# Kernel tuning notes

Measured on AMD Instinct MI355X. Metric: run time of the kernel, lower is better.

Reference implementation:

```python
import jax, jax.numpy as jnp
import numpy as np

N_NODES = 100000
N_EDGES = 1600000
N_GRAPHS = 512
IN_F, H1, H2 = 128, 128, 256
N_GROUPS, N_FAM = 16, 10


def setup_inputs() -> dict:
    key = jax.random.key(0)
    ks = jax.random.split(key, 8)
    x = jax.random.normal(ks[0], (N_NODES, IN_F), dtype=jnp.float32)
    edge_index = jax.random.randint(ks[1], (2, N_EDGES), 0, N_NODES, dtype=jnp.int64)
    batch = jnp.sort(jax.random.randint(ks[2], (N_NODES,), 0, N_GRAPHS, dtype=jnp.int64))
    W1 = jax.random.normal(ks[3], (IN_F, H1), dtype=jnp.float32) / np.sqrt(IN_F)
    b1 = jnp.zeros((H1,), dtype=jnp.float32)
    W2 = jax.random.normal(ks[4], (H1, H2), dtype=jnp.float32) / np.sqrt(H1)
    b2 = jnp.zeros((H2,), dtype=jnp.float32)
    Wg = jax.random.normal(ks[5], (H2, N_GROUPS), dtype=jnp.float32) / np.sqrt(H2)
    bg = jnp.zeros((N_GROUPS,), dtype=jnp.float32)
    Wf = jax.random.normal(ks[6], (N_GROUPS, H2, N_FAM), dtype=jnp.float32) / np.sqrt(H2)
    bf = jnp.zeros((N_GROUPS, N_FAM), dtype=jnp.float32)
    return {"x": x, "edge_index": edge_index, "batch": batch,
            "W1": W1, "b1": b1, "W2": W2, "b2": b2,
            "Wg": Wg, "bg": bg, "Wf": Wf, "bf": bf}


def gcn_conv(x, W, b, src, dst, num_nodes):
    # PyG GCNConv: add self-loops, symmetric normalization, scatter-add aggregation.
    xw = x @ W  # [N, out]
    deg = jax.ops.segment_sum(jnp.ones((src.shape[0],), x.dtype), dst,
                              num_segments=num_nodes) + 1.0  # +1 self-loop
    dinv = jax.lax.rsqrt(deg)
    coef = dinv[src] * dinv[dst]            # [E]
    msg = xw[src] * coef[:, None]           # gather + scale (memory-bound)
    agg = jax.ops.segment_sum(msg, dst, num_segments=num_nodes)
    agg = agg + xw * (dinv * dinv)[:, None]  # self-loop contribution
    return agg + b


def reference(x, edge_index, batch, W1, b1, W2, b2, Wg, bg, Wf, bf):
    src, dst = edge_index[0], edge_index[1]
    h = jax.nn.relu(gcn_conv(x, W1, b1, src, dst, N_NODES))
    # dropout p=0.5 is identity in eval mode
    h = gcn_conv(h, W2, b2, src, dst, N_NODES)
    # global mean pool over graphs
    sums = jax.ops.segment_sum(h, batch, num_segments=N_GRAPHS)       # [G, H2]
    cnts = jax.ops.segment_sum(jnp.ones((N_NODES,), h.dtype), batch,
                               num_segments=N_GRAPHS)
    pooled = sums / jnp.maximum(cnts, 1.0)[:, None]
    group_logits = pooled @ Wg + bg                                   # [G, num_groups]
    family_logits = jnp.einsum('bd,gdf->gbf', pooled, Wf) + bf[:, None, :]
    return group_logits, family_logits
```

## Files before the change

### kernel.cpp

```cpp
#include <hip/hip_runtime.h>

#define NN 100000
#define NE 1600000
#define NGR 512
#define KF 128
#define H2F 256
#define NGRP 16
#define NFAM 10

#define CH 128
#define NCHUNK ((NN + CH - 1) / CH)
#define PT 6656
#define NT ((NE + PT - 1) / PT)
#define PREPB_BLKS 64
#define GBB ((NN + 255) / 256)

#define NSPLIT 8
#define SRCMASK 0x1FFFF

typedef __attribute__((ext_vector_type(8))) short short8;
typedef __attribute__((ext_vector_type(4))) float floatx4;
typedef __attribute__((ext_vector_type(2))) float floatx2;

__device__ __forceinline__ unsigned short f2bf(float f) {
  unsigned u = __float_as_uint(f);
  unsigned r = (u + 0x7fff + ((u >> 16) & 1)) >> 16;
  return (unsigned short)r;
}
__device__ __forceinline__ unsigned short pk_fp8(float a, float b) {
  return (unsigned short)__builtin_amdgcn_cvt_pk_fp8_f32(a, b, 0, false);
}
__device__ __forceinline__ floatx2 unpk_fp8(unsigned short u) {
  return __builtin_amdgcn_cvt_pk_f32_fp8((int)u, false);
}


__global__ __launch_bounds__(256) void k_histprep(const int* __restrict__ ei,
                                                  const int* __restrict__ batch,
                                                  int* __restrict__ tot,
                                                  int* __restrict__ gb,
                                                  const float* __restrict__ W,
                                                  unsigned short* __restrict__ Bp) {
  __shared__ int lh[NCHUNK];
  int tid = threadIdx.x;
  if (blockIdx.x >= NT + PREPB_BLKS) {
    int n = (blockIdx.x - NT - PREPB_BLKS) * 256 + tid;
    if (n >= NN) return;
    int b0 = batch[n];
    if (n == 0) {
      for (int g = 0; g <= b0; ++g) gb[g] = 0;
    }
    int b1 = (n + 1 < NN) ? batch[n + 1] : NGR;
    for (int g = b0 + 1; g <= b1; ++g) gb[g] = n + 1;
    return;
  }
  if (blockIdx.x >= NT) {
    int idx = (blockIdx.x - NT) * 256 + tid;
    int j = idx & 7;
    int l = (idx >> 3) & 63;
    int rest = idx >> 9;
    int nc = rest & 7;
    int kc = rest >> 3;
    int k = kc * 32 + (l >> 4) * 8 + j;
    int nn = nc * 16 + (l & 15);
    Bp[idx] = f2bf(W[k * KF + nn]);
    return;
  }
  for (int g = tid; g < NCHUNK; g += 256) lh[g] = 0;
  __syncthreads();
  int base = blockIdx.x * PT;
  int nv = min(PT, NE - base);
  for (int i = tid; i < nv; i += 256) atomicAdd(&lh[ei[NE + base + i] >> 7], 1);
  __syncthreads();
  for (int g = tid; g < NCHUNK; g += 256) {
    int v = lh[g];
    if (v) atomicAdd(&tot[g], v);
  }
}


__global__ __launch_bounds__(256) void k_scantot(const int* __restrict__ tot,
                                                 int* __restrict__ cbase,
                                                 int* __restrict__ cursor) {
  __shared__ int ssc[256];
  int tid = threadIdx.x;
  int v4[4]; int loc = 0;
#pragma unroll
  for (int j = 0; j < 4; ++j) {
    int idx = tid * 4 + j;
    v4[j] = (idx < NCHUNK) ? tot[idx] : 0;
    loc += v4[j];
  }
  ssc[tid] = loc;
  __syncthreads();
  for (int off = 1; off < 256; off <<= 1) {
    int val = (tid >= off) ? ssc[tid - off] : 0;
    __syncthreads();
    ssc[tid] += val;
    __syncthreads();
  }
  int excl = ssc[tid] - loc;
#pragma unroll
  for (int j = 0; j < 4; ++j) {
    int idx = tid * 4 + j;
    if (idx < NCHUNK) { cbase[idx] = excl; cursor[idx] = excl; }
    excl += v4[j];
  }
  if (tid == 255) cbase[NCHUNK] = excl;
}


__global__ __launch_bounds__(256) void k_pscatter(const int* __restrict__ ei,
                                                  int* __restrict__ cursor,
                                                  int* __restrict__ erec) {
  __shared__ int stage[PT];
  __shared__ unsigned short stagec[PT];
  __shared__ int lstart[NCHUNK];
  __shared__ int lrun[NCHUNK];
  __shared__ int gbase[NCHUNK];
  __shared__ int ssc[256];
  int t0 = blockIdx.x, tid = threadIdx.x;
  for (int g = tid; g < NCHUNK; g += 256) lrun[g] = 0;
  __syncthreads();
  int base = t0 * PT;
  int nv = min(PT, NE - base);
  for (int i = tid; i < nv; i += 256) atomicAdd(&lrun[ei[NE + base + i] >> 7], 1);
  __syncthreads();
  int v4[4]; int loc = 0;
#pragma unroll
  for (int j = 0; j < 4; ++j) {
    int idx = tid * 4 + j;
    v4[j] = (idx < NCHUNK) ? lrun[idx] : 0;
    loc += v4[j];
  }
  ssc[tid] = loc;
  __syncthreads();
  for (int off = 1; off < 256; off <<= 1) {
    int val = (tid >= off) ? ssc[tid - off] : 0;
    __syncthreads();
    ssc[tid] += val;
    __syncthreads();
  }
  int excl = ssc[tid] - loc;
#pragma unroll
  for (int j = 0; j < 4; ++j) {
    int idx = tid * 4 + j;
    if (idx < NCHUNK) lstart[idx] = excl;
    excl += v4[j];
  }
  __syncthreads();
  for (int g = tid; g < NCHUNK; g += 256) {
    int cnt = ((g + 1 < NCHUNK) ? lstart[g + 1] : nv) - lstart[g];
    gbase[g] = cnt ? atomicAdd(&cursor[g], cnt) : 0;
    lrun[g] = lstart[g];
  }
  __syncthreads();
  for (int i = tid; i < nv; i += 256) {
    int s = ei[base + i], d = ei[NE + base + i];
    int g = d >> 7;
    int pos = atomicAdd(&lrun[g], 1);
    stage[pos] = ((d & (CH - 1)) << 17) | s;
    stagec[pos] = (unsigned short)g;
  }
  __syncthreads();
  for (int j = tid; j < nv; j += 256) {
    int g = stagec[j];
    erec[gbase[g] + (j - lstart[g])] = stage[j];
  }
}


__global__ __launch_bounds__(256) void k_sort(const int* __restrict__ erec,
                                              const int* __restrict__ cbase,
                                              int* __restrict__ esrc,
                                              int* __restrict__ rowptr,
                                              float* __restrict__ dinv) {
  __shared__ int hist[CH];
  __shared__ int lrun[CH];
  __shared__ int sc[256];
  const int c = blockIdx.x, tid = threadIdx.x;
  const int e0 = cbase[c], e1 = cbase[c + 1];
  const int nv = e1 - e0;
  if (tid < CH) hist[tid] = 0;
  __syncthreads();
  for (int i = tid; i < nv; i += 256) atomicAdd(&hist[(erec[e0 + i] >> 17) & (CH - 1)], 1);
  __syncthreads();
  int deg = (tid < CH) ? hist[tid] : 0;
  sc[tid] = deg;
  __syncthreads();
  for (int off = 1; off < 256; off <<= 1) {
    int val = (tid >= off) ? sc[tid - off] : 0;
    __syncthreads();
    sc[tid] += val;
    __syncthreads();
  }
  int excl = sc[tid] - deg;
  int node = c * CH + tid;
  if (tid < CH) {
    lrun[tid] = excl;
    if (node < NN) {
      rowptr[node] = e0 + excl;
      dinv[node] = rsqrtf((float)(deg + 1));
    } else if (node == NN) {
      rowptr[NN] = e0 + excl;
    }
  }
  __syncthreads();
  for (int i = tid; i < nv; i += 256) {
    int r = erec[e0 + i];
    int pos = atomicAdd(&lrun[(r >> 17) & (CH - 1)], 1);
    esrc[e0 + pos] = r & SRCMASK;
  }
}


__global__ __launch_bounds__(256) void k_gemm_mfma(const float* __restrict__ A,
                                                   const unsigned short* __restrict__ Bp,
                                                   const float* __restrict__ dinv,
                                                   unsigned short* __restrict__ C) {
  constexpr int K = 128;
  constexpr int NCH = KF / 16;
  const int wv = blockIdx.x * 4 + (threadIdx.x >> 6);
  const int row0 = wv * 16;
  if (row0 >= NN) return;
  const int lane = threadIdx.x & 63;
  const int m = lane & 15;
  const int q = lane >> 4;

  floatx4 acc[NCH];
#pragma unroll
  for (int i = 0; i < NCH; ++i) acc[i] = (floatx4){0.f, 0.f, 0.f, 0.f};

  const int arow = row0 + m;
#pragma unroll
  for (int kc = 0; kc < 4; ++kc) {
    const float* ap = A + (size_t)arow * K + kc * 32 + q * 8;
    float4 f0 = *(const float4*)ap;
    float4 f1 = *(const float4*)(ap + 4);
    short8 af;
    af[0] = (short)f2bf(f0.x); af[1] = (short)f2bf(f0.y);
    af[2] = (short)f2bf(f0.z); af[3] = (short)f2bf(f0.w);
    af[4] = (short)f2bf(f1.x); af[5] = (short)f2bf(f1.y);
    af[6] = (short)f2bf(f1.z); af[7] = (short)f2bf(f1.w);
    const unsigned short* bp = Bp + (size_t)kc * NCH * 512;
#pragma unroll
    for (int nc = 0; nc < NCH; ++nc) {
      short8 bfr = *(const short8*)(bp + (size_t)nc * 512 + lane * 8);
      acc[nc] = __builtin_amdgcn_mfma_f32_16x16x32_bf16(af, bfr, acc[nc], 0, 0, 0);
    }
  }

  float ds[4];
#pragma unroll
  for (int r = 0; r < 4; ++r) ds[r] = dinv[row0 + q * 4 + r];
#pragma unroll
  for (int nc = 0; nc < 4; ++nc) {
#pragma unroll
    for (int r = 0; r < 4; ++r) {
      int row = row0 + q * 4 + r;
      C[(size_t)row * 64 + nc * 16 + m] =
          pk_fp8(acc[nc][r] * ds[r], acc[nc + 4][r] * ds[r]);
    }
  }
}


__global__ __launch_bounds__(128) void k_agg1(const unsigned short* __restrict__ p,
                                              const float* __restrict__ bias,
                                              const int* __restrict__ rowptr,
                                              const int* __restrict__ esrc,
                                              const float* __restrict__ dinv,
                                              unsigned short* __restrict__ outp) {
  const int n = blockIdx.x * 2 + (threadIdx.x >> 6);
  const int t = threadIdx.x & 63;
  const int u = t & 31;
  const int half = t >> 5;
  const unsigned* __restrict__ prow = (const unsigned*)p;

  float a0 = 0.f, a1 = 0.f, a2 = 0.f, a3 = 0.f;

  if (half == 0) {
    unsigned v = prow[((unsigned)n << 5) + u];
    floatx2 lo = unpk_fp8((unsigned short)(v & 0xffffu));
    floatx2 hi = unpk_fp8((unsigned short)(v >> 16));
    a0 = lo.x; a1 = lo.y; a2 = hi.x; a3 = hi.y;
  }

  const int r0 = rowptr[n];
  const int r1 = rowptr[n + 1];
  int i = r0;

#define PAIR_TIER(NP)                                                  \
  for (; i + 2 * (NP) <= r1; i += 2 * (NP)) {                          \
    const int ib = i + half;                                           \
    unsigned s[NP];                                                    \
    _Pragma("unroll") for (int j = 0; j < (NP); ++j)                   \
        s[j] = (unsigned)esrc[ib + 2 * j];                             \
    unsigned v[NP];                                                    \
    _Pragma("unroll") for (int j = 0; j < (NP); ++j)                   \
        v[j] = prow[(s[j] << 5) + u];                                  \
    _Pragma("unroll") for (int j = 0; j < (NP); ++j) {                 \
      floatx2 lo = unpk_fp8((unsigned short)(v[j] & 0xffffu));         \
      floatx2 hi = unpk_fp8((unsigned short)(v[j] >> 16));             \
      a0 += lo.x; a1 += lo.y; a2 += hi.x; a3 += hi.y;                  \
    }                                                                  \
  }

  PAIR_TIER(8)
  PAIR_TIER(4)
  PAIR_TIER(2)
  PAIR_TIER(1)
#undef PAIR_TIER

  if (i < r1 && half == 0) {
    unsigned s = (unsigned)esrc[i];
    unsigned v = prow[(s << 5) + u];
    floatx2 lo = unpk_fp8((unsigned short)(v & 0xffffu));
    floatx2 hi = unpk_fp8((unsigned short)(v >> 16));
    a0 += lo.x; a1 += lo.y; a2 += hi.x; a3 += hi.y;
  }

  a0 += __shfl_down(a0, 32, 64);
  a1 += __shfl_down(a1, 32, 64);
  a2 += __shfl_down(a2, 32, 64);
  a3 += __shfl_down(a3, 32, 64);

  if (half == 0) {
    const float dn = dinv[n];
    float2 blo = *(const float2*)(bias + 2 * u);
    float2 bhi = *(const float2*)(bias + 64 + 2 * u);
    float x0 = fmaxf(fmaf(dn, a0, blo.x), 0.f) * dn;
    float x1 = fmaxf(fmaf(dn, a1, bhi.x), 0.f) * dn;
    float x2 = fmaxf(fmaf(dn, a2, blo.y), 0.f) * dn;
    float x3 = fmaxf(fmaf(dn, a3, bhi.y), 0.f) * dn;
    unsigned lo = pk_fp8(x0, x1);
    unsigned hi = pk_fp8(x2, x3);
    ((unsigned*)outp)[((unsigned)n << 5) + u] = lo | (hi << 16);
  }
}


__global__ __launch_bounds__(256) void k_aggpart(const unsigned short* __restrict__ p,
                                                 const int* __restrict__ gb,
                                                 const int* __restrict__ rowptr,
                                                 const int* __restrict__ esrc,
                                                 const float* __restrict__ dinv,
                                                 float* __restrict__ pooled) {
  __shared__ float sacc[4][128];
  const int g = blockIdx.x / NSPLIT;
  const int part = blockIdx.x % NSPLIT;
  const int tid = threadIdx.x;
  const int start = gb[g], end = gb[g + 1];
  const int wv = tid >> 6, t = tid & 63, u = t & 31, half = t >> 5;
  const unsigned* __restrict__ prow = (const unsigned*)p;

  float a0 = 0.f, a1 = 0.f, a2 = 0.f, a3 = 0.f;

  const int nlen = end - start;
  const int nper = (nlen + NSPLIT - 1) / NSPLIT;
  const int ns = min(start + part * nper, end);
  const int ne = min(ns + nper, end);

  for (int n = ns + wv; n < ne; n += 4) {
    float t0, t1, t2, t3;
    if (half == 0) {
      unsigned v = prow[((unsigned)n << 5) + u];
      floatx2 lo = unpk_fp8((unsigned short)(v & 0xffffu));
      floatx2 hi = unpk_fp8((unsigned short)(v >> 16));
      t0 = lo.x; t1 = lo.y; t2 = hi.x; t3 = hi.y;
    } else {
      t0 = 0.f; t1 = 0.f; t2 = 0.f; t3 = 0.f;
    }
    const int r0 = rowptr[n];
    const int r1 = rowptr[n + 1];
    int i = r0;

#define PAIR_TIER(NP)                                                  \
    for (; i + 2 * (NP) <= r1; i += 2 * (NP)) {                        \
      const int ib = i + half;                                         \
      unsigned s[NP];                                                  \
      _Pragma("unroll") for (int j = 0; j < (NP); ++j)                 \
          s[j] = (unsigned)esrc[ib + 2 * j];                           \
      unsigned v[NP];                                                  \
      _Pragma("unroll") for (int j = 0; j < (NP); ++j)                 \
          v[j] = prow[(s[j] << 5) + u];                                \
      _Pragma("unroll") for (int j = 0; j < (NP); ++j) {               \
        floatx2 lo = unpk_fp8((unsigned short)(v[j] & 0xffffu));       \
        floatx2 hi = unpk_fp8((unsigned short)(v[j] >> 16));           \
        t0 += lo.x; t1 += lo.y; t2 += hi.x; t3 += hi.y;                \
      }                                                                \
    }

    PAIR_TIER(8)
    PAIR_TIER(4)
    PAIR_TIER(2)
    PAIR_TIER(1)
#undef PAIR_TIER

    if (i < r1 && half == 0) {
      unsigned s = (unsigned)esrc[i];
      unsigned v = prow[(s << 5) + u];
      floatx2 lo = unpk_fp8((unsigned short)(v & 0xffffu));
      floatx2 hi = unpk_fp8((unsigned short)(v >> 16));
      t0 += lo.x; t1 += lo.y; t2 += hi.x; t3 += hi.y;
    }

    const float dn = dinv[n];
    a0 = fmaf(dn, t0, a0); a1 = fmaf(dn, t1, a1);
    a2 = fmaf(dn, t2, a2); a3 = fmaf(dn, t3, a3);
  }

  a0 += __shfl_down(a0, 32, 64);
  a1 += __shfl_down(a1, 32, 64);
  a2 += __shfl_down(a2, 32, 64);
  a3 += __shfl_down(a3, 32, 64);
  if (half == 0) {
    sacc[wv][2 * u] = a0;
    sacc[wv][2 * u + 1] = a2;
    sacc[wv][2 * u + 64] = a1;
    sacc[wv][2 * u + 65] = a3;
  }
  __syncthreads();
  if (tid < KF) {
    float v = sacc[0][tid] + sacc[1][tid] + sacc[2][tid] + sacc[3][tid];
    atomicAdd(&pooled[(size_t)g * KF + tid], v);
  }
}


__global__ __launch_bounds__(256) void k_heads(const float* __restrict__ pooled,
                                               const int* __restrict__ gb,
                                               const float* __restrict__ W2,
                                               const float* __restrict__ b2,
                                               const float* __restrict__ Wg,
                                               const float* __restrict__ bg,
                                               const float* __restrict__ Wf,
                                               const float* __restrict__ bfb,
                                               float* __restrict__ out) {
  __shared__ float pr[KF];
  __shared__ float pp[H2F];
  const int g = blockIdx.x;
  const int tid = threadIdx.x;
  if (tid < KF) {
    float c = fmaxf((float)(gb[g + 1] - gb[g]), 1.f);
    pr[tid] = pooled[(size_t)g * KF + tid] / c;
  }
  __syncthreads();
  float acc = b2[tid];
#pragma unroll 8
  for (int d = 0; d < KF; ++d) acc = fmaf(pr[d], W2[d * H2F + tid], acc);
  pp[tid] = acc;
  __syncthreads();
  if (tid < NGRP) {
    float a = bg[tid];
    for (int d = 0; d < H2F; ++d) a = fmaf(pp[d], Wg[d * NGRP + tid], a);
    out[g * NGRP + tid] = a;
  } else if (tid >= 64 && tid < 64 + NGRP * NFAM) {
    int uu = tid - 64;
    int gg = uu / NFAM;
    int ff = uu % NFAM;
    float a = bfb[gg * NFAM + ff];
    for (int d = 0; d < H2F; ++d) a = fmaf(pp[d], Wf[(gg * H2F + d) * NFAM + ff], a);
    out[NGR * NGRP + (size_t)gg * NGR * NFAM + g * NFAM + ff] = a;
  }
}


extern "C" void kernel_launch(void* const* d_in, const int* in_sizes, int n_in,
                              void* d_out, int out_size, void* d_ws, size_t ws_size,
                              hipStream_t stream) {
  const float* x    = (const float*)d_in[0];
  const int*   ei   = (const int*)d_in[1];
  const int*   batch= (const int*)d_in[2];
  const float* W1   = (const float*)d_in[3];
  const float* b1   = (const float*)d_in[4];
  const float* W2   = (const float*)d_in[5];
  const float* b2   = (const float*)d_in[6];
  const float* Wg   = (const float*)d_in[7];
  const float* bg   = (const float*)d_in[8];
  const float* Wf   = (const float*)d_in[9];
  const float* bfb  = (const float*)d_in[10];
  float* out = (float*)d_out;

  char* w = (char*)d_ws;
  auto take = [&](size_t bytes) {
    char* p = w;
    w += (bytes + 255) & ~(size_t)255;
    return (void*)p;
  };
  int*   tot   = (int*)take((size_t)NCHUNK * 4);
  float* pooled= (float*)take((size_t)NGR * KF * 4);
  int*   gb    = (int*)take((size_t)(NGR + 1) * 4);
  int*   cbase = (int*)take((size_t)(NCHUNK + 1) * 4);
  int*   cursor= (int*)take((size_t)NCHUNK * 4);
  int*   erec  = (int*)take((size_t)NE * 4);
  int*   esrc  = (int*)take((size_t)NE * 4);
  int*   rowptr= (int*)take((size_t)(NN + 1) * 4);
  float* dinv  = (float*)take((size_t)NN * 4);
  unsigned short* Bp1 = (unsigned short*)take((size_t)KF * KF * 2);
  unsigned short* xw1 = (unsigned short*)take((size_t)NN * 64 * 2);
  unsigned short* h1  = (unsigned short*)take((size_t)NN * 64 * 2);

  size_t zbytes = (size_t)((char*)pooled - (char*)tot) + (size_t)NGR * KF * 4;
  hipMemsetAsync(tot, 0, zbytes, stream);

  k_histprep<<<NT + PREPB_BLKS + GBB, 256, 0, stream>>>(ei, batch, tot, gb, W1, Bp1);
  k_scantot<<<1, 256, 0, stream>>>(tot, cbase, cursor);
  k_pscatter<<<NT, 256, 0, stream>>>(ei, cursor, erec);
  k_sort<<<NCHUNK, 256, 0, stream>>>(erec, cbase, esrc, rowptr, dinv);

  k_gemm_mfma<<<1563, 256, 0, stream>>>(x, Bp1, dinv, xw1);

  k_agg1<<<NN / 2, 128, 0, stream>>>(xw1, b1, rowptr, esrc, dinv, h1);
  k_aggpart<<<NGR * NSPLIT, 256, 0, stream>>>(h1, gb, rowptr, esrc, dinv, pooled);
  k_heads<<<NGR, 256, 0, stream>>>(pooled, gb, W2, b2, Wg, bg, Wf, bfb, out);
}
```

Before: 292.1 us.

## Compute degrees early and co-launch GEMM with partition scatter

Per-node in-degrees are now counted with global atomics in the histogram kernel, and dinv is computed in the scan kernel instead of in the sort kernel. Because dinv is ready sooner, the first-layer MFMA GEMM no longer has to wait for the sort. It is merged into the partition-scatter launch as extra blocks, so GEMM work overlaps the scatter and one kernel launch is removed. The cost is 1.6M extra global atomics on a 100K-entry degree array and a larger memset. The GEMM blocks also now carry the scatter kernel's large shared-memory footprint, which may lower their occupancy.

```diff
diff --git a/kernel.cpp b/kernel.cpp
--- a/kernel.cpp
+++ b/kernel.cpp
@@ -14,6 +14,7 @@
 #define NT ((NE + PT - 1) / PT)
 #define PREPB_BLKS 64
 #define GBB ((NN + 255) / 256)
+#define GEMMB 1563
 
 #define NSPLIT 8
 #define SRCMASK 0x1FFFF
@@ -38,6 +39,7 @@
 __global__ __launch_bounds__(256) void k_histprep(const int* __restrict__ ei,
                                                   const int* __restrict__ batch,
                                                   int* __restrict__ tot,
+                                                  int* __restrict__ nodedeg,
                                                   int* __restrict__ gb,
                                                   const float* __restrict__ W,
                                                   unsigned short* __restrict__ Bp) {
@@ -70,7 +72,11 @@
   __syncthreads();
   int base = blockIdx.x * PT;
   int nv = min(PT, NE - base);
-  for (int i = tid; i < nv; i += 256) atomicAdd(&lh[ei[NE + base + i] >> 7], 1);
+  for (int i = tid; i < nv; i += 256) {
+    int d = ei[NE + base + i];
+    atomicAdd(&lh[d >> 7], 1);
+    atomicAdd(&nodedeg[d], 1);
+  }
   __syncthreads();
   for (int g = tid; g < NCHUNK; g += 256) {
     int v = lh[g];
@@ -79,11 +85,18 @@
 }
 
 
-__global__ __launch_bounds__(256) void k_scantot(const int* __restrict__ tot,
-                                                 int* __restrict__ cbase,
-                                                 int* __restrict__ cursor) {
+__global__ __launch_bounds__(256) void k_scandinv(const int* __restrict__ tot,
+                                                  int* __restrict__ cbase,
+                                                  int* __restrict__ cursor,
+                                                  const int* __restrict__ nodedeg,
+                                                  float* __restrict__ dinv) {
+  int tid = threadIdx.x;
+  if (blockIdx.x > 0) {
+    int n = (blockIdx.x - 1) * 256 + tid;
+    if (n < NN) dinv[n] = rsqrtf((float)(nodedeg[n] + 1));
+    return;
+  }
   __shared__ int ssc[256];
-  int tid = threadIdx.x;
   int v4[4]; int loc = 0;
 #pragma unroll
   for (int j = 0; j < 4; ++j) {
@@ -110,16 +123,70 @@
 }
 
 
-__global__ __launch_bounds__(256) void k_pscatter(const int* __restrict__ ei,
-                                                  int* __restrict__ cursor,
-                                                  int* __restrict__ erec) {
+__global__ __launch_bounds__(256) void k_pscgemm(const int* __restrict__ ei,
+                                                 int* __restrict__ cursor,
+                                                 int* __restrict__ erec,
+                                                 const float* __restrict__ A,
+                                                 const unsigned short* __restrict__ Bp,
+                                                 const float* __restrict__ dinv,
+                                                 unsigned short* __restrict__ C) {
   __shared__ int stage[PT];
   __shared__ unsigned short stagec[PT];
   __shared__ int lstart[NCHUNK];
   __shared__ int lrun[NCHUNK];
   __shared__ int gbase[NCHUNK];
   __shared__ int ssc[256];
-  int t0 = blockIdx.x, tid = threadIdx.x;
+  const int tid = threadIdx.x;
+
+  if (blockIdx.x >= NT) {
+    constexpr int K = 128;
+    constexpr int NCH = KF / 16;
+    const int wv = (blockIdx.x - NT) * 4 + (tid >> 6);
+    const int row0 = wv * 16;
+    if (row0 >= NN) return;
+    const int lane = tid & 63;
+    const int m = lane & 15;
+    const int q = lane >> 4;
+
+    floatx4 acc[NCH];
+#pragma unroll
+    for (int i = 0; i < NCH; ++i) acc[i] = (floatx4){0.f, 0.f, 0.f, 0.f};
+
+    const int arow = row0 + m;
+#pragma unroll
+    for (int kc = 0; kc < 4; ++kc) {
+      const float* ap = A + (size_t)arow * K + kc * 32 + q * 8;
+      float4 f0 = *(const float4*)ap;
+      float4 f1 = *(const float4*)(ap + 4);
+      short8 af;
+      af[0] = (short)f2bf(f0.x); af[1] = (short)f2bf(f0.y);
+      af[2] = (short)f2bf(f0.z); af[3] = (short)f2bf(f0.w);
+      af[4] = (short)f2bf(f1.x); af[5] = (short)f2bf(f1.y);
+      af[6] = (short)f2bf(f1.z); af[7] = (short)f2bf(f1.w);
+      const unsigned short* bp = Bp + (size_t)kc * NCH * 512;
+#pragma unroll
+      for (int nc = 0; nc < NCH; ++nc) {
+        short8 bfr = *(const short8*)(bp + (size_t)nc * 512 + lane * 8);
+        acc[nc] = __builtin_amdgcn_mfma_f32_16x16x32_bf16(af, bfr, acc[nc], 0, 0, 0);
+      }
+    }
+
+    float ds[4];
+#pragma unroll
+    for (int r = 0; r < 4; ++r) ds[r] = dinv[row0 + q * 4 + r];
+#pragma unroll
+    for (int nc = 0; nc < 4; ++nc) {
+#pragma unroll
+      for (int r = 0; r < 4; ++r) {
+        int row = row0 + q * 4 + r;
+        C[(size_t)row * 64 + nc * 16 + m] =
+            pk_fp8(acc[nc][r] * ds[r], acc[nc + 4][r] * ds[r]);
+      }
+    }
+    return;
+  }
+
+  int t0 = blockIdx.x;
   for (int g = tid; g < NCHUNK; g += 256) lrun[g] = 0;
   __syncthreads();
   int base = t0 * PT;
@@ -173,8 +240,7 @@
 __global__ __launch_bounds__(256) void k_sort(const int* __restrict__ erec,
                                               const int* __restrict__ cbase,
                                               int* __restrict__ esrc,
-                                              int* __restrict__ rowptr,
-                                              float* __restrict__ dinv) {
+                                              int* __restrict__ rowptr) {
   __shared__ int hist[CH];
   __shared__ int lrun[CH];
   __shared__ int sc[256];
@@ -200,7 +266,6 @@
     lrun[tid] = excl;
     if (node < NN) {
       rowptr[node] = e0 + excl;
-      dinv[node] = rsqrtf((float)(deg + 1));
     } else if (node == NN) {
       rowptr[NN] = e0 + excl;
     }
@@ -210,57 +275,6 @@
     int r = erec[e0 + i];
     int pos = atomicAdd(&lrun[(r >> 17) & (CH - 1)], 1);
     esrc[e0 + pos] = r & SRCMASK;
-  }
-}
-
-
-__global__ __launch_bounds__(256) void k_gemm_mfma(const float* __restrict__ A,
-                                                   const unsigned short* __restrict__ Bp,
-                                                   const float* __restrict__ dinv,
-                                                   unsigned short* __restrict__ C) {
-  constexpr int K = 128;
-  constexpr int NCH = KF / 16;
-  const int wv = blockIdx.x * 4 + (threadIdx.x >> 6);
-  const int row0 = wv * 16;
-  if (row0 >= NN) return;
-  const int lane = threadIdx.x & 63;
-  const int m = lane & 15;
-  const int q = lane >> 4;
-
-  floatx4 acc[NCH];
-#pragma unroll
-  for (int i = 0; i < NCH; ++i) acc[i] = (floatx4){0.f, 0.f, 0.f, 0.f};
-
-  const int arow = row0 + m;
-#pragma unroll
-  for (int kc = 0; kc < 4; ++kc) {
-    const float* ap = A + (size_t)arow * K + kc * 32 + q * 8;
-    float4 f0 = *(const float4*)ap;
-    float4 f1 = *(const float4*)(ap + 4);
-    short8 af;
-    af[0] = (short)f2bf(f0.x); af[1] = (short)f2bf(f0.y);
-    af[2] = (short)f2bf(f0.z); af[3] = (short)f2bf(f0.w);
-    af[4] = (short)f2bf(f1.x); af[5] = (short)f2bf(f1.y);
-    af[6] = (short)f2bf(f1.z); af[7] = (short)f2bf(f1.w);
-    const unsigned short* bp = Bp + (size_t)kc * NCH * 512;
-#pragma unroll
-    for (int nc = 0; nc < NCH; ++nc) {
-      short8 bfr = *(const short8*)(bp + (size_t)nc * 512 + lane * 8);
-      acc[nc] = __builtin_amdgcn_mfma_f32_16x16x32_bf16(af, bfr, acc[nc], 0, 0, 0);
-    }
-  }
-
-  float ds[4];
-#pragma unroll
-  for (int r = 0; r < 4; ++r) ds[r] = dinv[row0 + q * 4 + r];
-#pragma unroll
-  for (int nc = 0; nc < 4; ++nc) {
-#pragma unroll
-    for (int r = 0; r < 4; ++r) {
-      int row = row0 + q * 4 + r;
-      C[(size_t)row * 64 + nc * 16 + m] =
-          pk_fp8(acc[nc][r] * ds[r], acc[nc + 4][r] * ds[r]);
-    }
   }
 }
 
@@ -488,28 +502,27 @@
     w += (bytes + 255) & ~(size_t)255;
     return (void*)p;
   };
-  int*   tot   = (int*)take((size_t)NCHUNK * 4);
-  float* pooled= (float*)take((size_t)NGR * KF * 4);
-  int*   gb    = (int*)take((size_t)(NGR + 1) * 4);
-  int*   cbase = (int*)take((size_t)(NCHUNK + 1) * 4);
-  int*   cursor= (int*)take((size_t)NCHUNK * 4);
-  int*   erec  = (int*)take((size_t)NE * 4);
-  int*   esrc  = (int*)take((size_t)NE * 4);
-  int*   rowptr= (int*)take((size_t)(NN + 1) * 4);
-  float* dinv  = (float*)take((size_t)NN * 4);
+  int*   tot    = (int*)take((size_t)NCHUNK * 4);
+  float* pooled = (float*)take((size_t)NGR * KF * 4);
+  int*   nodedeg= (int*)take((size_t)NN * 4);
+  int*   gb     = (int*)take((size_t)(NGR + 1) * 4);
+  int*   cbase  = (int*)take((size_t)(NCHUNK + 1) * 4);
+  int*   cursor = (int*)take((size_t)NCHUNK * 4);
+  int*   erec   = (int*)take((size_t)NE * 4);
+  int*   esrc   = (int*)take((size_t)NE * 4);
+  int*   rowptr = (int*)take((size_t)(NN + 1) * 4);
+  float* dinv   = (float*)take((size_t)NN * 4);
   unsigned short* Bp1 = (unsigned short*)take((size_t)KF * KF * 2);
   unsigned short* xw1 = (unsigned short*)take((size_t)NN * 64 * 2);
   unsigned short* h1  = (unsigned short*)take((size_t)NN * 64 * 2);
 
-  size_t zbytes = (size_t)((char*)pooled - (char*)tot) + (size_t)NGR * KF * 4;
+  size_t zbytes = (size_t)((char*)nodedeg - (char*)tot) + (size_t)NN * 4;
   hipMemsetAsync(tot, 0, zbytes, stream);
 
-  k_histprep<<<NT + PREPB_BLKS + GBB, 256, 0, stream>>>(ei, batch, tot, gb, W1, Bp1);
-  k_scantot<<<1, 256, 0, stream>>>(tot, cbase, cursor);
-  k_pscatter<<<NT, 256, 0, stream>>>(ei, cursor, erec);
-  k_sort<<<NCHUNK, 256, 0, stream>>>(erec, cbase, esrc, rowptr, dinv);
-
-  k_gemm_mfma<<<1563, 256, 0, stream>>>(x, Bp1, dinv, xw1);
+  k_histprep<<<NT + PREPB_BLKS + GBB, 256, 0, stream>>>(ei, batch, tot, nodedeg, gb, W1, Bp1);
+  k_scandinv<<<1 + GBB, 256, 0, stream>>>(tot, cbase, cursor, nodedeg, dinv);
+  k_pscgemm<<<NT + GEMMB, 256, 0, stream>>>(ei, cursor, erec, x, Bp1, dinv, xw1);
+  k_sort<<<NCHUNK, 256, 0, stream>>>(erec, cbase, esrc, rowptr);
 
   k_agg1<<<NN / 2, 128, 0, stream>>>(xw1, b1, rowptr, esrc, dinv, h1);
   k_aggpart<<<NGR * NSPLIT, 256, 0, stream>>>(h1, gb, rowptr, esrc, dinv, pooled);
```

After: 333.7 us. +14.2%, slower.
